# Kernel tuning notes

Hardware: AMD Instinct MI355X
Metric: run time of the kernel (lower is better)

Reference implementation:

```python
import jax, jax.numpy as jnp
import numpy as np

B, TH, TS, HS, WS = 16, 1024, 1024, 1024, 1024


def setup_inputs() -> dict:
    key = jax.random.key(0)
    k1, k2, k3, k4 = jax.random.split(key, 4)
    h = jax.random.normal(k1, (B, TH, HS), dtype=jnp.float32)
    s = jax.random.normal(k2, (B, TS, WS), dtype=jnp.float32)
    # nn.Linear params: weight [out, in], bias [out]
    Wh = jax.random.normal(k3, (HS, HS), dtype=jnp.float32) * 0.02
    bh = jnp.zeros((HS,), dtype=jnp.float32)
    Ws = jax.random.normal(k4, (HS, WS), dtype=jnp.float32) * 0.02
    bs = jnp.zeros((HS,), dtype=jnp.float32)
    return {"h": h, "s": s, "Wh": Wh, "bh": bh, "Ws": Ws, "bs": bs}


def reference(h, s, Wh, bh, Ws, bs):
    hp = jnp.einsum('bth,oh->bto', h, Wh) + bh          # [B, TH, HS]
    sp = jnp.einsum('btw,ow->bto', s, Ws) + bs          # [B, TS, HS]
    scores = jnp.einsum('bik,bjk->bij', hp, sp)         # [B, TH, TS]
    b, th, _ = scores.shape
    # faithful to torch: flat-chunk into rows of length TH, softmax over dim 1
    sm = jax.nn.softmax(scores.reshape(-1, th), axis=1).reshape(b, -1, th)  # [B, TS, TH]
    res = jnp.matmul(sm, hp)                            # [B, TS, HS]
    return res.reshape(-1, res.shape[-1])               # [B*TS, HS]
```

## Files before the change

### kernel.cpp

```cpp
#include <hip/hip_runtime.h>
#include <hip/hip_bf16.h>
#include <stdint.h>


typedef _Float16 half_t;
typedef __attribute__((ext_vector_type(8))) _Float16 half8;
typedef __attribute__((ext_vector_type(4))) _Float16 half4;
typedef __attribute__((ext_vector_type(4))) float floatx4;

__device__ __forceinline__ void gl2lds16(const void* g, void* l) {
    __builtin_amdgcn_global_load_lds(
        (const __attribute__((address_space(1))) uint32_t*)(uintptr_t)g,
        (__attribute__((address_space(3))) uint32_t*)(uintptr_t)l,
        16, 0, 0);
}

#define NT16 16

template<int WF32, int WH16, int WH16T, int RSA, int SWZ>
__global__ __launch_bounds__(512, 2) void gemm256(
    const half_t* __restrict__ A, const float* __restrict__ A32,
    const half_t* __restrict__ B,
    const float* __restrict__ bias,
    float* __restrict__ Cf, half_t* __restrict__ Ch, half_t* __restrict__ ChT,
    int lda, int ldb, int N,
    long aBatch, long bBatch, long cfBatch, int ldcf)
{
    extern __shared__ char smem[];

    const int tid  = threadIdx.x;
    const int wave = tid >> 6;
    const int lane = tid & 63;
    const int wr = wave >> 2;
    const int wc = wave & 3;
    const int lr = lane & 15, lg = lane >> 4;

    long batch; int row0, col0;
    if constexpr (SWZ) {
        const int lin = blockIdx.x + (blockIdx.y << 2) + (blockIdx.z << 4);
        const int xcd = lin & 7, per = lin >> 3;
        batch = (xcd << 1) | (per >> 4);
        const int wt = per & 15;
        row0 = (wt & 3) * 256;
        col0 = (wt >> 2) * 256;
    } else {
        batch = blockIdx.z;
        row0 = blockIdx.x * 256;
        col0 = blockIdx.y * 256;
    }

    const half_t* Bb = B + batch * bBatch;

    floatx4 acc[8][4];
#pragma unroll
    for (int m = 0; m < 8; ++m)
#pragma unroll
        for (int n = 0; n < 4; ++n)
            acc[m][n] = (floatx4){0.f, 0.f, 0.f, 0.f};

    long bOff[2][2];
    long aOffG[2][2];
#pragma unroll
    for (int hh = 0; hh < 2; ++hh)
#pragma unroll
        for (int i = 0; i < 2; ++i) {
            const int off = hh * 16384 + i * 8192 + tid * 16;
            const int e = off ^ (((off >> 7) & 7) << 4);
            const int r = e >> 7, cb = e & 127;
            bOff[hh][i] = (long)(col0 + r) * (long)(ldb * 2) + cb;
            if constexpr (!RSA)
                aOffG[hh][i] = (long)(row0 + r) * (long)(lda * 2) + cb;
        }

    const int wave_s = __builtin_amdgcn_readfirstlane(wave);
    auto stageB = [&](int buf, int kk) {
#pragma unroll
        for (int hh = 0; hh < 2; ++hh)
#pragma unroll
            for (int i = 0; i < 2; ++i)
                gl2lds16((const char*)Bb + bOff[hh][i] + (long)kk * 2,
                         smem + buf * 65536 + 32768 + hh * 16384 + i * 8192 + wave_s * 1024);
    };
    auto stageA16 = [&](int buf, int kk) {
        const half_t* Ab = A + batch * aBatch;
#pragma unroll
        for (int hh = 0; hh < 2; ++hh)
#pragma unroll
            for (int i = 0; i < 2; ++i)
                gl2lds16((const char*)Ab + aOffG[hh][i] + (long)kk * 2,
                         smem + buf * 65536 + hh * 16384 + i * 8192 + wave_s * 1024);
    };

    int rsaRow[4], rsaKb[4];
#pragma unroll
    for (int c = 0; c < 4; ++c) {
        const int off = c * 8192 + tid * 16;
        rsaRow[c] = off >> 7;
        rsaKb[c]  = off & 127;
    }

    uint32_t aof0 = (uint32_t)((wr * 128 + lr) * 128 + ((lg * 16) ^ ((lr & 7) << 4)));
    uint32_t aof1 = (uint32_t)((wr * 128 + lr) * 128 + ((64 + lg * 16) ^ ((lr & 7) << 4)));
    uint32_t bof0 = (uint32_t)(32768 + (wc * 64 + lr) * 128 + ((lg * 16) ^ ((lr & 7) << 4)));
    uint32_t bof1 = (uint32_t)(32768 + (wc * 64 + lr) * 128 + ((64 + lg * 16) ^ ((lr & 7) << 4)));

    auto rsaLoad = [&](float4 (&fv)[4][2], int kk) {
#pragma unroll
        for (int c = 0; c < 4; ++c) {
            const float* src = A32 + batch * aBatch
                             + (long)(row0 + rsaRow[c]) * lda + kk + (rsaKb[c] >> 1);
            fv[c][0] = *(const float4*)src;
            fv[c][1] = *(const float4*)(src + 4);
        }
    };
    auto rsaWrite = [&](float4 (&fv)[4][2], int buf) {
#pragma unroll
        for (int c = 0; c < 4; ++c) {
            half8 o = { (half_t)fv[c][0].x, (half_t)fv[c][0].y, (half_t)fv[c][0].z, (half_t)fv[c][0].w,
                        (half_t)fv[c][1].x, (half_t)fv[c][1].y, (half_t)fv[c][1].z, (half_t)fv[c][1].w };
            *(half8*)(smem + buf * 65536 + rsaRow[c] * 128
                      + (rsaKb[c] ^ ((rsaRow[c] & 7) << 4))) = o;
        }
    };

    if constexpr (RSA) {
        float4 fv[4][2];
        rsaLoad(fv, 0);
        stageB(0, 0);
        rsaWrite(fv, 0);
    } else {
        stageA16(0, 0);
        stageB(0, 0);
    }
    __syncthreads();

    for (int t = 0; t < NT16; ++t) {
        const int nxt = (t & 1) ^ 1;
        const int k1 = (t + 1) * 64;

        float4 fv[4][2];
        if (t + 1 < NT16) {
            if constexpr (RSA) {
                rsaLoad(fv, k1);
                stageB(nxt, k1);
            } else {
                stageA16(nxt, k1);
                stageB(nxt, k1);
            }
        }

        half8 aF[4][2], bF[4][2];
#pragma unroll
        for (int ni = 0; ni < 4; ++ni) {
            bF[ni][0] = *(const half8*)(smem + bof0 + ni * 2048);
            bF[ni][1] = *(const half8*)(smem + bof1 + ni * 2048);
        }
#pragma unroll
        for (int mi = 0; mi < 4; ++mi) {
            aF[mi][0] = *(const half8*)(smem + aof0 + mi * 2048);
            aF[mi][1] = *(const half8*)(smem + aof1 + mi * 2048);
        }

        if (RSA && t + 1 < NT16) rsaWrite(fv, nxt);

#pragma unroll
        for (int mi = 0; mi < 4; ++mi)
#pragma unroll
            for (int ni = 0; ni < 4; ++ni)
#pragma unroll
                for (int ks = 0; ks < 2; ++ks)
                    acc[mi][ni] = __builtin_amdgcn_mfma_f32_16x16x32_f16(
                        aF[mi][ks], bF[ni][ks], acc[mi][ni], 0, 0, 0);
#pragma unroll
        for (int mi = 0; mi < 4; ++mi) {
            aF[mi][0] = *(const half8*)(smem + aof0 + (4 + mi) * 2048);
            aF[mi][1] = *(const half8*)(smem + aof1 + (4 + mi) * 2048);
        }
#pragma unroll
        for (int mi = 0; mi < 4; ++mi)
#pragma unroll
            for (int ni = 0; ni < 4; ++ni)
#pragma unroll
                for (int ks = 0; ks < 2; ++ks)
                    acc[4 + mi][ni] = __builtin_amdgcn_mfma_f32_16x16x32_f16(
                        aF[mi][ks], bF[ni][ks], acc[4 + mi][ni], 0, 0, 0);

        __syncthreads();
        aof0 ^= 65536; aof1 ^= 65536; bof0 ^= 65536; bof1 ^= 65536;
    }

    {
        float* wlds = (float*)(smem + wave * 2304);
        float bv[4];
#pragma unroll
        for (int n = 0; n < 4; ++n)
            bv[n] = bias ? bias[col0 + wc * 64 + n * 16 + lr] : 0.f;
        const int er = lane >> 2, ec = lane & 3;
        const int oc = lane >> 1, tc = lane & 1;
#pragma unroll
        for (int m = 0; m < 8; ++m) {
#pragma unroll
            for (int np = 0; np < 2; ++np) {
#pragma unroll
                for (int n2 = 0; n2 < 2; ++n2)
#pragma unroll
                    for (int j = 0; j < 4; ++j)
                        wlds[(lg * 4 + j) * 36 + n2 * 16 + lr] =
                            acc[m][np * 2 + n2][j] + bv[np * 2 + n2];
                const int grow = row0 + wr * 128 + m * 16;
                const int gcol = col0 + wc * 64 + np * 32;
                float4 q0 = *(float4*)&wlds[er * 36 + ec * 8];
                float4 q1 = *(float4*)&wlds[er * 36 + ec * 8 + 4];
                if (WF32) {
                    float* p = Cf + batch * cfBatch + (long)(grow + er) * ldcf + gcol + ec * 8;
                    *(float4*)p = q0;
                    *(float4*)(p + 4) = q1;
                }
                if (WH16) {
                    half8 o = { (half_t)q0.x, (half_t)q0.y, (half_t)q0.z, (half_t)q0.w,
                                (half_t)q1.x, (half_t)q1.y, (half_t)q1.z, (half_t)q1.w };
                    *(half8*)&Ch[batch * cfBatch + (long)(grow + er) * N + gcol + ec * 8] = o;
                }
                if (WH16T) {
                    float tv[8];
#pragma unroll
                    for (int k = 0; k < 8; ++k)
                        tv[k] = wlds[(tc * 8 + k) * 36 + oc];
                    half8 o = { (half_t)tv[0], (half_t)tv[1], (half_t)tv[2], (half_t)tv[3],
                                (half_t)tv[4], (half_t)tv[5], (half_t)tv[6], (half_t)tv[7] };
                    const int gt = grow + tc * 8;
                    *(half8*)&ChT[(long)(gt >> 10) * 1048576
                                  + (long)(gcol + oc) * 1024 + (gt & 1023)] = o;
                }
                __builtin_amdgcn_s_waitcnt(0);
            }
        }
    }
}

__global__ void softmax_h(half_t* __restrict__ S) {
    const long r = blockIdx.x;
    half_t* row = S + r * 1024;
    const int tid = threadIdx.x;
    const int wave = tid >> 6, lane = tid & 63;

    half4 h4 = ((const half4*)row)[tid];
    float v0 = (float)h4[0], v1 = (float)h4[1], v2 = (float)h4[2], v3 = (float)h4[3];
    float mx = fmaxf(fmaxf(v0, v1), fmaxf(v2, v3));
#pragma unroll
    for (int off = 32; off > 0; off >>= 1)
        mx = fmaxf(mx, __shfl_xor(mx, off));
    __shared__ float rmx[4], rsm[4];
    if (lane == 0) rmx[wave] = mx;
    __syncthreads();
    mx = fmaxf(fmaxf(rmx[0], rmx[1]), fmaxf(rmx[2], rmx[3]));

    float e0 = __expf(v0 - mx), e1 = __expf(v1 - mx);
    float e2 = __expf(v2 - mx), e3 = __expf(v3 - mx);
    float s = e0 + e1 + e2 + e3;
#pragma unroll
    for (int off = 32; off > 0; off >>= 1)
        s += __shfl_xor(s, off);
    if (lane == 0) rsm[wave] = s;
    __syncthreads();
    s = rsm[0] + rsm[1] + rsm[2] + rsm[3];

    const float inv = 1.0f / s;
    half4 o = { (half_t)(e0 * inv), (half_t)(e1 * inv), (half_t)(e2 * inv), (half_t)(e3 * inv) };
    ((half4*)row)[tid] = o;
}

__global__ void cvt_f16(const float4* __restrict__ src, half4* __restrict__ dst, int n4) {
    const int stride = gridDim.x * blockDim.x;
    for (int i = blockIdx.x * blockDim.x + threadIdx.x; i < n4; i += stride) {
        float4 v = src[i];
        half4 o = { (half_t)v.x, (half_t)v.y, (half_t)v.z, (half_t)v.w };
        dst[i] = o;
    }
}

extern "C" void kernel_launch(void* const* d_in, const int* in_sizes, int n_in,
                              void* d_out, int out_size, void* d_ws, size_t ws_size,
                              hipStream_t stream) {
    const float* h  = (const float*)d_in[0];
    const float* s  = (const float*)d_in[1];
    const float* Wh = (const float*)d_in[2];
    const float* bh = (const float*)d_in[3];
    const float* Ws = (const float*)d_in[4];
    const float* bs = (const float*)d_in[5];

    const long MB = 16384;
    const long D  = 1024;

    char* w = (char*)d_ws;
    half_t* sc16 = (half_t*)w;  w += MB * D * 2;
    half_t* Wh16 = (half_t*)w;  w += D * D * 2;
    half_t* Ws16 = (half_t*)w;  w += D * D * 2;
    half_t* hp16 = (half_t*)w;  w += MB * D * 2;
    half_t* sp16 = (half_t*)w;  w += MB * D * 2;
    half_t* hpT  = (half_t*)w;  w += MB * D * 2;

    (void)hipFuncSetAttribute(reinterpret_cast<const void*>(&gemm256<0,1,1,1,0>),
                        hipFuncAttributeMaxDynamicSharedMemorySize, 131072);
    (void)hipFuncSetAttribute(reinterpret_cast<const void*>(&gemm256<0,1,0,1,0>),
                        hipFuncAttributeMaxDynamicSharedMemorySize, 131072);
    (void)hipFuncSetAttribute(reinterpret_cast<const void*>(&gemm256<0,1,0,0,1>),
                        hipFuncAttributeMaxDynamicSharedMemorySize, 131072);
    (void)hipFuncSetAttribute(reinterpret_cast<const void*>(&gemm256<1,0,0,0,1>),
                        hipFuncAttributeMaxDynamicSharedMemorySize, 131072);

    cvt_f16<<<512, 256, 0, stream>>>((const float4*)Wh, (half4*)Wh16, (int)(D * D / 4));
    cvt_f16<<<512, 256, 0, stream>>>((const float4*)Ws, (half4*)Ws16, (int)(D * D / 4));

    gemm256<0,1,1,1,0><<<dim3(64, 4, 1), 512, 131072, stream>>>(
        nullptr, h, Wh16, bh, nullptr, hp16, hpT, 1024, 1024, 1024, 0, 0, 0, 0);
    gemm256<0,1,0,1,0><<<dim3(64, 4, 1), 512, 131072, stream>>>(
        nullptr, s, Ws16, bs, nullptr, sp16, nullptr, 1024, 1024, 1024, 0, 0, 0, 0);
    gemm256<0,1,0,0,1><<<dim3(4, 4, 16), 512, 131072, stream>>>(
        hp16, nullptr, sp16, nullptr, nullptr, sc16, nullptr, 1024, 1024, 1024,
        1048576L, 1048576L, 1048576L, 0);
    softmax_h<<<16384, 256, 0, stream>>>(sc16);
    gemm256<1,0,0,0,1><<<dim3(4, 4, 16), 512, 131072, stream>>>(
        sc16, nullptr, hpT, nullptr, (float*)d_out, nullptr, nullptr,
        1024, 1024, 1024, 1048576L, 1048576L, 1048576L, 1024);
}
```

Measured before the change: 216.1 us.

## Pre-convert h and s to fp16 with XCD-pinned block mapping for L2 locality

Replaces the in-GEMM fp32-to-fp16 register staging of h and s with a separate conversion kernel that writes fp16 copies, so the projection GEMMs can use direct global-to-LDS async loads for both operands. The conversion kernel, the projection GEMM tile mapping and the softmax row mapping are remapped so that each XCD (selected by block index mod 8) works on a contiguous slice of rows, which is meant to keep the fp16 intermediates resident in that XCD's L2 between kernels. This adds an extra pass over h and s plus extra workspace and two launches, in exchange for a simpler, fully asynchronous load path in the GEMM.

```diff
diff --git a/kernel.cpp b/kernel.cpp
--- a/kernel.cpp
+++ b/kernel.cpp
@@ -17,10 +17,9 @@
 
 #define NT16 16
 
-template<int WF32, int WH16, int WH16T, int RSA, int SWZ>
+template<int WF32, int WH16, int WH16T, int SWZ, int PIN>
 __global__ __launch_bounds__(512, 2) void gemm256(
-    const half_t* __restrict__ A, const float* __restrict__ A32,
-    const half_t* __restrict__ B,
+    const half_t* __restrict__ A, const half_t* __restrict__ B,
     const float* __restrict__ bias,
     float* __restrict__ Cf, half_t* __restrict__ Ch, half_t* __restrict__ ChT,
     int lda, int ldb, int N,
@@ -43,12 +42,19 @@
         const int wt = per & 15;
         row0 = (wt & 3) * 256;
         col0 = (wt >> 2) * 256;
+    } else if constexpr (PIN) {
+        const int lin = blockIdx.x + (blockIdx.y << 6);
+        const int q = lin >> 3;
+        batch = 0;
+        row0 = (8 * (lin & 7) + (q & 7)) * 256;
+        col0 = (q >> 3) * 256;
     } else {
         batch = blockIdx.z;
         row0 = blockIdx.x * 256;
         col0 = blockIdx.y * 256;
     }
 
+    const half_t* Ab = A + batch * aBatch;
     const half_t* Bb = B + batch * bBatch;
 
     floatx4 acc[8][4];
@@ -58,8 +64,7 @@
         for (int n = 0; n < 4; ++n)
             acc[m][n] = (floatx4){0.f, 0.f, 0.f, 0.f};
 
-    long bOff[2][2];
-    long aOffG[2][2];
+    long aOff[2][2], bOff[2][2];
 #pragma unroll
     for (int hh = 0; hh < 2; ++hh)
 #pragma unroll
@@ -67,13 +72,18 @@
             const int off = hh * 16384 + i * 8192 + tid * 16;
             const int e = off ^ (((off >> 7) & 7) << 4);
             const int r = e >> 7, cb = e & 127;
+            aOff[hh][i] = (long)(row0 + r) * (long)(lda * 2) + cb;
             bOff[hh][i] = (long)(col0 + r) * (long)(ldb * 2) + cb;
-            if constexpr (!RSA)
-                aOffG[hh][i] = (long)(row0 + r) * (long)(lda * 2) + cb;
         }
 
     const int wave_s = __builtin_amdgcn_readfirstlane(wave);
-    auto stageB = [&](int buf, int kk) {
+    auto stage = [&](int buf, int kk) {
+#pragma unroll
+        for (int hh = 0; hh < 2; ++hh)
+#pragma unroll
+            for (int i = 0; i < 2; ++i)
+                gl2lds16((const char*)Ab + aOff[hh][i] + (long)kk * 2,
+                         smem + buf * 65536 + hh * 16384 + i * 8192 + wave_s * 1024);
 #pragma unroll
         for (int hh = 0; hh < 2; ++hh)
 #pragma unroll
@@ -81,73 +91,17 @@
                 gl2lds16((const char*)Bb + bOff[hh][i] + (long)kk * 2,
                          smem + buf * 65536 + 32768 + hh * 16384 + i * 8192 + wave_s * 1024);
     };
-    auto stageA16 = [&](int buf, int kk) {
-        const half_t* Ab = A + batch * aBatch;
-#pragma unroll
-        for (int hh = 0; hh < 2; ++hh)
-#pragma unroll
-            for (int i = 0; i < 2; ++i)
-                gl2lds16((const char*)Ab + aOffG[hh][i] + (long)kk * 2,
-                         smem + buf * 65536 + hh * 16384 + i * 8192 + wave_s * 1024);
-    };
-
-    int rsaRow[4], rsaKb[4];
-#pragma unroll
-    for (int c = 0; c < 4; ++c) {
-        const int off = c * 8192 + tid * 16;
-        rsaRow[c] = off >> 7;
-        rsaKb[c]  = off & 127;
-    }
 
     uint32_t aof0 = (uint32_t)((wr * 128 + lr) * 128 + ((lg * 16) ^ ((lr & 7) << 4)));
     uint32_t aof1 = (uint32_t)((wr * 128 + lr) * 128 + ((64 + lg * 16) ^ ((lr & 7) << 4)));
     uint32_t bof0 = (uint32_t)(32768 + (wc * 64 + lr) * 128 + ((lg * 16) ^ ((lr & 7) << 4)));
     uint32_t bof1 = (uint32_t)(32768 + (wc * 64 + lr) * 128 + ((64 + lg * 16) ^ ((lr & 7) << 4)));
 
-    auto rsaLoad = [&](float4 (&fv)[4][2], int kk) {
-#pragma unroll
-        for (int c = 0; c < 4; ++c) {
-            const float* src = A32 + batch * aBatch
-                             + (long)(row0 + rsaRow[c]) * lda + kk + (rsaKb[c] >> 1);
-            fv[c][0] = *(const float4*)src;
-            fv[c][1] = *(const float4*)(src + 4);
-        }
-    };
-    auto rsaWrite = [&](float4 (&fv)[4][2], int buf) {
-#pragma unroll
-        for (int c = 0; c < 4; ++c) {
-            half8 o = { (half_t)fv[c][0].x, (half_t)fv[c][0].y, (half_t)fv[c][0].z, (half_t)fv[c][0].w,
-                        (half_t)fv[c][1].x, (half_t)fv[c][1].y, (half_t)fv[c][1].z, (half_t)fv[c][1].w };
-            *(half8*)(smem + buf * 65536 + rsaRow[c] * 128
-                      + (rsaKb[c] ^ ((rsaRow[c] & 7) << 4))) = o;
-        }
-    };
-
-    if constexpr (RSA) {
-        float4 fv[4][2];
-        rsaLoad(fv, 0);
-        stageB(0, 0);
-        rsaWrite(fv, 0);
-    } else {
-        stageA16(0, 0);
-        stageB(0, 0);
-    }
+    stage(0, 0);
     __syncthreads();
 
     for (int t = 0; t < NT16; ++t) {
-        const int nxt = (t & 1) ^ 1;
-        const int k1 = (t + 1) * 64;
-
-        float4 fv[4][2];
-        if (t + 1 < NT16) {
-            if constexpr (RSA) {
-                rsaLoad(fv, k1);
-                stageB(nxt, k1);
-            } else {
-                stageA16(nxt, k1);
-                stageB(nxt, k1);
-            }
-        }
+        if (t + 1 < NT16) stage((t & 1) ^ 1, (t + 1) * 64);
 
         half8 aF[4][2], bF[4][2];
 #pragma unroll
@@ -160,9 +114,6 @@
             aF[mi][0] = *(const half8*)(smem + aof0 + mi * 2048);
             aF[mi][1] = *(const half8*)(smem + aof1 + mi * 2048);
         }
-
-        if (RSA && t + 1 < NT16) rsaWrite(fv, nxt);
-
 #pragma unroll
         for (int mi = 0; mi < 4; ++mi)
 #pragma unroll
@@ -239,7 +190,8 @@
 }
 
 __global__ void softmax_h(half_t* __restrict__ S) {
-    const long r = blockIdx.x;
+    const long l = blockIdx.x;
+    const long r = 2048 * (l & 7) + (l >> 3);
     half_t* row = S + r * 1024;
     const int tid = threadIdx.x;
     const int wave = tid >> 6, lane = tid & 63;
@@ -268,6 +220,18 @@
     const float inv = 1.0f / s;
     half4 o = { (half_t)(e0 * inv), (half_t)(e1 * inv), (half_t)(e2 * inv), (half_t)(e3 * inv) };
     ((half4*)row)[tid] = o;
+}
+
+__global__ void cvt_pin(const float4* __restrict__ src, half4* __restrict__ dst) {
+    const int l = blockIdx.x;
+    const long base = (2048L * (l & 7) + 8L * (l >> 3)) * 256;
+    const int tid = threadIdx.x;
+#pragma unroll
+    for (int k = 0; k < 8; ++k) {
+        float4 v = src[base + k * 256 + tid];
+        half4 o = { (half_t)v.x, (half_t)v.y, (half_t)v.z, (half_t)v.w };
+        dst[base + k * 256 + tid] = o;
+    }
 }
 
 __global__ void cvt_f16(const float4* __restrict__ src, half4* __restrict__ dst, int n4) {
@@ -296,31 +260,37 @@
     half_t* sc16 = (half_t*)w;  w += MB * D * 2;
     half_t* Wh16 = (half_t*)w;  w += D * D * 2;
     half_t* Ws16 = (half_t*)w;  w += D * D * 2;
+    half_t* h16  = (half_t*)w;  w += MB * D * 2;
+    half_t* s16  = (half_t*)w;  w += MB * D * 2;
     half_t* hp16 = (half_t*)w;  w += MB * D * 2;
     half_t* sp16 = (half_t*)w;  w += MB * D * 2;
     half_t* hpT  = (half_t*)w;  w += MB * D * 2;
 
-    (void)hipFuncSetAttribute(reinterpret_cast<const void*>(&gemm256<0,1,1,1,0>),
+    (void)hipFuncSetAttribute(reinterpret_cast<const void*>(&gemm256<0,1,1,0,1>),
+                        hipFuncAttributeMaxDynamicSharedMemorySize, 131072);
+    (void)hipFuncSetAttribute(reinterpret_cast<const void*>(&gemm256<0,1,0,0,1>),
                         hipFuncAttributeMaxDynamicSharedMemorySize, 131072);
     (void)hipFuncSetAttribute(reinterpret_cast<const void*>(&gemm256<0,1,0,1,0>),
                         hipFuncAttributeMaxDynamicSharedMemorySize, 131072);
-    (void)hipFuncSetAttribute(reinterpret_cast<const void*>(&gemm256<0,1,0,0,1>),
-                        hipFuncAttributeMaxDynamicSharedMemorySize, 131072);
-    (void)hipFuncSetAttribute(reinterpret_cast<const void*>(&gemm256<1,0,0,0,1>),
+    (void)hipFuncSetAttribute(reinterpret_cast<const void*>(&gemm256<1,0,0,1,0>),
                         hipFuncAttributeMaxDynamicSharedMemorySize, 131072);
 
     cvt_f16<<<512, 256, 0, stream>>>((const float4*)Wh, (half4*)Wh16, (int)(D * D / 4));
     cvt_f16<<<512, 256, 0, stream>>>((const float4*)Ws, (half4*)Ws16, (int)(D * D / 4));
 
-    gemm256<0,1,1,1,0><<<dim3(64, 4, 1), 512, 131072, stream>>>(
-        nullptr, h, Wh16, bh, nullptr, hp16, hpT, 1024, 1024, 1024, 0, 0, 0, 0);
-    gemm256<0,1,0,1,0><<<dim3(64, 4, 1), 512, 131072, stream>>>(
-        nullptr, s, Ws16, bs, nullptr, sp16, nullptr, 1024, 1024, 1024, 0, 0, 0, 0);
-    gemm256<0,1,0,0,1><<<dim3(4, 4, 16), 512, 131072, stream>>>(
-        hp16, nullptr, sp16, nullptr, nullptr, sc16, nullptr, 1024, 1024, 1024,
+    cvt_pin<<<2048, 256, 0, stream>>>((const float4*)h, (half4*)h16);
+    gemm256<0,1,1,0,1><<<dim3(64, 4, 1), 512, 131072, stream>>>(
+        h16, Wh16, bh, nullptr, hp16, hpT, 1024, 1024, 1024, 0, 0, 0, 0);
+
+    cvt_pin<<<2048, 256, 0, stream>>>((const float4*)s, (half4*)s16);
+    gemm256<0,1,0,0,1><<<dim3(64, 4, 1), 512, 131072, stream>>>(
+        s16, Ws16, bs, nullptr, sp16, nullptr, 1024, 1024, 1024, 0, 0, 0, 0);
+
+    gemm256<0,1,0,1,0><<<dim3(4, 4, 16), 512, 131072, stream>>>(
+        hp16, sp16, nullptr, nullptr, sc16, nullptr, 1024, 1024, 1024,
         1048576L, 1048576L, 1048576L, 0);
     softmax_h<<<16384, 256, 0, stream>>>(sc16);
-    gemm256<1,0,0,0,1><<<dim3(4, 4, 16), 512, 131072, stream>>>(
-        sc16, nullptr, hpT, nullptr, (float*)d_out, nullptr, nullptr,
+    gemm256<1,0,0,1,0><<<dim3(4, 4, 16), 512, 131072, stream>>>(
+        sc16, hpT, nullptr, (float*)d_out, nullptr, nullptr,
         1024, 1024, 1024, 1048576L, 1048576L, 1048576L, 1024);
 }
```

Result: slower. 228.3 us (+5.6%).
